# Performance work log

Hardware: AMD Instinct MI355X
Metric: run time of the kernel (lower is better)

The kernel has to match this reference:

```python
import jax, jax.numpy as jnp
from jax import lax
import numpy as np

B, T, F = 256, 2048, 12
EV_VOCAB, RS_VOCAB = 32, 8
EED, RED = 6, 3
H, K = 96, 3
D = F + EED + RED  # 21


def setup_inputs() -> dict:
    key = jax.random.key(0)
    ks = jax.random.split(key, 12)
    s = 0.05
    return {
        'seq': jax.random.normal(ks[0], (B, T, F), jnp.float32),
        'ev': jax.random.randint(ks[1], (B, T), 0, EV_VOCAB),
        'rs': jax.random.randint(ks[2], (B, T), 0, RS_VOCAB),
        'lengths': jax.random.randint(ks[3], (B,), 1, T + 1),  # valid lengths in [1, T]
        'event_emb': jax.random.normal(ks[4], (EV_VOCAB, EED), jnp.float32) * s,
        'result_emb': jax.random.normal(ks[5], (RS_VOCAB, RED), jnp.float32) * s,
        'W_ih': jax.random.normal(ks[6], (4 * H, D), jnp.float32) * s,
        'W_hh': jax.random.normal(ks[7], (4 * H, H), jnp.float32) * s,
        'b_ih': jnp.zeros((4 * H,), jnp.float32),
        'b_hh': jnp.zeros((4 * H,), jnp.float32),
        'W_mlp': jax.random.normal(ks[8], (H, H * K), jnp.float32) * s,
        'b_mlp': jnp.zeros((H,), jnp.float32),
        'W_fc': jax.random.normal(ks[9], (2, 2 * H), jnp.float32) * s,
        'b_fc': jnp.zeros((2,), jnp.float32),
    }


def reference(seq, ev, rs, lengths, event_emb, result_emb, W_ih, W_hh, b_ih, b_hh,
              W_mlp, b_mlp, W_fc, b_fc):
    # embed + concat -> [B,T,D]
    x = jnp.concatenate([seq, event_emb[ev], result_emb[rs]], axis=-1)
    xs = jnp.swapaxes(x, 0, 1)  # [T,B,D]
    ts = jnp.arange(T)
    b = b_ih + b_hh

    def step(carry, inp):
        h, c = carry
        x_t, t = inp
        gates = x_t @ W_ih.T + h @ W_hh.T + b  # [B,4H]
        i, f, g, o = jnp.split(gates, 4, axis=-1)  # PyTorch gate order i,f,g,o
        i = jax.nn.sigmoid(i); f = jax.nn.sigmoid(f)
        g = jnp.tanh(g); o = jax.nn.sigmoid(o)
        c_new = f * c + i * g
        h_new = o * jnp.tanh(c_new)
        m = (t < lengths)[:, None]  # packed-seq semantics: freeze state past length
        h = jnp.where(m, h_new, h)
        c = jnp.where(m, c_new, c)
        out = jnp.where(m, h_new, jnp.zeros_like(h_new))  # pad_packed zeros
        return (h, c), out

    h0 = jnp.zeros((B, H), x.dtype)
    (h_fin, _), outs = lax.scan(step, (h0, h0), (xs, ts))
    out_padded = jnp.swapaxes(outs, 0, 1)  # [B,T,H]

    # vectorized last-k gather (replaces torch Python loop)
    idx = lengths[:, None] - K + jnp.arange(K)  # [B,K]
    valid = idx >= 0
    gathered = jnp.take_along_axis(out_padded, jnp.clip(idx, 0)[:, :, None], axis=1)
    gathered = jnp.where(valid[:, :, None], gathered, jnp.zeros_like(gathered))
    lastk = gathered.reshape(B, K * H)

    h_lastk = jax.nn.relu(lastk @ W_mlp.T + b_mlp)
    h = jnp.concatenate([h_fin, h_lastk], axis=1)  # [B,2H]
    return h @ W_fc.T + b_fc  # [B,2]
```

## Files before the change

kernel.cpp:

```cpp
#include <hip/hip_runtime.h>

#define TT 2048
#define FF 12
#define HH 96
#define CH 128
#define L2E 1.44269504088896340736f

__device__ __forceinline__ float fast_exp2(float x){ return __builtin_amdgcn_exp2f(x); }
__device__ __forceinline__ float fast_rcp(float x){ return __builtin_amdgcn_rcpf(x); }

__global__ __launch_bounds__(512, 2) void lstm_persist(
  const float* __restrict__ seq, const int* __restrict__ ev, const int* __restrict__ rsi,
  const int* __restrict__ len, const float* __restrict__ eemb, const float* __restrict__ remb,
  const float* __restrict__ W_ih, const float* __restrict__ W_hh,
  const float* __restrict__ b_ih, const float* __restrict__ b_hh,
  const float* __restrict__ W_mlp, const float* __restrict__ b_mlp,
  const float* __restrict__ W_fc, const float* __restrict__ b_fc,
  float* __restrict__ out)
{
  const int b   = blockIdx.x;
  const int tid = threadIdx.x;
  const int w   = tid >> 6;
  const int l   = tid & 63;

  __shared__ __align__(16) float vh[HH];
  __shared__ __align__(16) float xch[CH][32];
  __shared__ __align__(16) float part[6*8*64];
  __shared__ __align__(16) float act[384];
  __shared__ __align__(16) float lastk[3*HH];
  __shared__ __align__(16) float h2[2*HH];
  __shared__ __align__(16) float et[32*6];
  __shared__ __align__(16) float rt[8*3];
  __shared__ int evb[CH];
  __shared__ int rsb[CH];

  float wreg[96];
  if (w < 6) {
    #pragma unroll
    for (int k = 0; k < 6; ++k) {
      const int g = l + 64*k;
      const float* p = W_hh + g*96 + 16*w;
      #pragma unroll
      for (int i = 0; i < 16; ++i) wreg[k*16+i] = p[i];
    }
  } else if (w == 6) {
    #pragma unroll
    for (int k = 0; k < 6; ++k) {
      const int g = l + 64*k;
      const float* p = W_ih + g*21;
      #pragma unroll
      for (int i = 0; i < 16; ++i) wreg[k*16+i] = p[i];
    }
  } else {
    #pragma unroll
    for (int k = 0; k < 6; ++k) {
      const int g = l + 64*k;
      #pragma unroll
      for (int i = 0; i < 16; ++i) {
        const int c = 16 + i;
        wreg[k*16+i] = (c < 21) ? W_ih[g*21 + c] : 0.f;
      }
    }
  }
  const float bg = (tid < 384) ? (b_ih[tid] + b_hh[tid]) : 0.f;

  for (int i = tid; i < HH;   i += 512) vh[i] = 0.f;
  for (int i = tid; i < 3*HH; i += 512) lastk[i] = 0.f;
  for (int i = tid; i < 192;  i += 512) et[i] = eemb[i];
  for (int i = tid; i < 24;   i += 512) rt[i] = remb[i];

  float c_state = 0.f;
  const int L = len[b];

  for (int t0 = 0; t0 < L; t0 += CH) {
    for (int q = tid; q < CH*FF; q += 512) {
      const int r = q / 12;
      const int c = q - r*12;
      xch[r][c] = seq[(size_t)b*(TT*FF) + (size_t)t0*FF + q];
    }
    if (tid < CH) {
      evb[tid] = ev [b*TT + t0 + tid];
      rsb[tid] = rsi[b*TT + t0 + tid];
    }
    __syncthreads();
    for (int q = tid; q < CH*20; q += 512) {
      const int r  = q / 20;
      const int cc = q - r*20 + 12;
      float val;
      if (cc < 18)      val = et[evb[r]*6 + (cc-12)];
      else if (cc < 21) val = rt[rsb[r]*3 + (cc-18)];
      else              val = 0.f;
      xch[r][cc] = val;
    }
    __syncthreads();

    const int nr = min(CH, L - t0);
    for (int r = 0; r < nr; ++r) {
      const float* sp = (w < 6) ? (vh + 16*w) : (&xch[r][16*(w-6)]);
      const float4 q0 = ((const float4*)sp)[0];
      const float4 q1 = ((const float4*)sp)[1];
      const float4 q2 = ((const float4*)sp)[2];
      const float4 q3 = ((const float4*)sp)[3];
      const float xv[16] = {q0.x,q0.y,q0.z,q0.w, q1.x,q1.y,q1.z,q1.w,
                            q2.x,q2.y,q2.z,q2.w, q3.x,q3.y,q3.z,q3.w};
      #pragma unroll
      for (int k = 0; k < 6; ++k) {
        float a = 0.f;
        #pragma unroll
        for (int i = 0; i < 16; ++i) a = fmaf(wreg[k*16+i], xv[i], a);
        part[(k*8 + w)*64 + l] = a;
      }
      __syncthreads();
      if (tid < 384) {
        float s = bg;
        const int kk = tid >> 6;
        const int ll = tid & 63;
        #pragma unroll
        for (int ww = 0; ww < 8; ++ww) s += part[(kk*8 + ww)*64 + ll];
        const bool is_t = (tid >= 192) && (tid < 288);
        const float arg = is_t ? (-2.f*L2E)*fabsf(s) : (-L2E)*s;
        const float e  = fast_exp2(arg);
        const float r1 = fast_rcp(1.f + e);
        const float th = copysignf((1.f - e) * r1, s);
        act[tid] = is_t ? th : r1;
      }
      __syncthreads();
      if (tid < 96) {
        const float i_ = act[tid];
        const float f_ = act[96  + tid];
        const float g_ = act[192 + tid];
        const float o_ = act[288 + tid];
        c_state = fmaf(f_, c_state, i_*g_);
        const float e  = fast_exp2((-2.f*L2E)*fabsf(c_state));
        const float th = copysignf((1.f - e) * fast_rcp(1.f + e), c_state);
        const float hn = o_ * th;
        vh[tid] = hn;
        const int kk = (t0 + r) + 3 - L;
        if (kk >= 0) lastk[kk*96 + tid] = hn;
      }
      __syncthreads();
    }
  }

  if (tid < 192) {
    const int hh = tid / 96;
    const int m  = tid - hh*96;
    const float* wp = W_mlp + m*288 + hh*144;
    const float* xp = lastk + hh*144;
    float s = 0.f;
    #pragma unroll 8
    for (int i = 0; i < 144; ++i) s = fmaf(wp[i], xp[i], s);
    act[tid] = s;
  }
  __syncthreads();
  if (tid < 96) {
    const float hl = act[tid] + act[96+tid] + b_mlp[tid];
    h2[96 + tid] = fmaxf(hl, 0.f);
    h2[tid] = vh[tid];
  }
  __syncthreads();
  if (tid < 128) {
    const int o  = tid >> 6;
    const int ll = tid & 63;
    const float* wf = W_fc + o*192 + 3*ll;
    float s = fmaf(wf[0], h2[3*ll+0], fmaf(wf[1], h2[3*ll+1], wf[2]*h2[3*ll+2]));
    #pragma unroll
    for (int off = 32; off > 0; off >>= 1) s += __shfl_down(s, off);
    if (ll == 0) out[b*2 + o] = s + b_fc[o];
  }
}

extern "C" void kernel_launch(void* const* d_in, const int* in_sizes, int n_in,
                              void* d_out, int out_size, void* d_ws, size_t ws_size,
                              hipStream_t stream) {
  const float* seq   = (const float*)d_in[0];
  const int*   ev    = (const int*)  d_in[1];
  const int*   rsi   = (const int*)  d_in[2];
  const int*   len   = (const int*)  d_in[3];
  const float* eemb  = (const float*)d_in[4];
  const float* remb  = (const float*)d_in[5];
  const float* W_ih  = (const float*)d_in[6];
  const float* W_hh  = (const float*)d_in[7];
  const float* b_ih  = (const float*)d_in[8];
  const float* b_hh  = (const float*)d_in[9];
  const float* W_mlp = (const float*)d_in[10];
  const float* b_mlp = (const float*)d_in[11];
  const float* W_fc  = (const float*)d_in[12];
  const float* b_fc  = (const float*)d_in[13];

  hipLaunchKernelGGL(lstm_persist, dim3(256), dim3(512), 0, stream,
                     seq, ev, rsi, len, eemb, remb, W_ih, W_hh, b_ih, b_hh,
                     W_mlp, b_mlp, W_fc, b_fc, (float*)d_out);
}
```

Baseline: 1.327 ms.

## Restructure LSTM step to one barrier using in-wave gate exchange and double-buffered h

Each thread now owns one gate row split across two half-waves, using 60 packed weights and f2 FMAs. Gate partial sums are combined with a shuffle, and the i/f/g/o activations are exchanged among lanes with shuffles. This replaces the shared-memory partial reduction and activation buffers and removes two of the three barriers per timestep. Double-buffering h avoids a read/write race with only one barrier per step, and the block grows to 768 threads. The cost is redundant cell-state computation across lanes.

```diff
diff --git a/kernel.cpp b/kernel.cpp
--- a/kernel.cpp
+++ b/kernel.cpp
@@ -4,12 +4,16 @@
 #define FF 12
 #define HH 96
 #define CH 128
+#define NT 768
 #define L2E 1.44269504088896340736f
+
+typedef __attribute__((ext_vector_type(2))) float f2;
+typedef __attribute__((ext_vector_type(4))) float f4;
 
 __device__ __forceinline__ float fast_exp2(float x){ return __builtin_amdgcn_exp2f(x); }
 __device__ __forceinline__ float fast_rcp(float x){ return __builtin_amdgcn_rcpf(x); }
 
-__global__ __launch_bounds__(512, 2) void lstm_persist(
+__global__ __launch_bounds__(NT, 3) void lstm_persist(
   const float* __restrict__ seq, const int* __restrict__ ev, const int* __restrict__ rsi,
   const int* __restrict__ len, const float* __restrict__ eemb, const float* __restrict__ remb,
   const float* __restrict__ W_ih, const float* __restrict__ W_hh,
@@ -22,58 +26,45 @@
   const int tid = threadIdx.x;
   const int w   = tid >> 6;
   const int l   = tid & 63;
+  const int kh  = l >> 5;
+  const int lh  = l & 31;
+  const int gt  = lh >> 3;
+  const int hq  = lh & 7;
+  const int ht  = 8*w + hq;
+  const int g   = gt*96 + ht;
 
-  __shared__ __align__(16) float vh[HH];
+  __shared__ __align__(16) float hbuf[2][96];
   __shared__ __align__(16) float xch[CH][32];
-  __shared__ __align__(16) float part[6*8*64];
-  __shared__ __align__(16) float act[384];
   __shared__ __align__(16) float lastk[3*HH];
+  __shared__ __align__(16) float tmp[192];
   __shared__ __align__(16) float h2[2*HH];
   __shared__ __align__(16) float et[32*6];
   __shared__ __align__(16) float rt[8*3];
   __shared__ int evb[CH];
   __shared__ int rsb[CH];
 
-  float wreg[96];
-  if (w < 6) {
-    #pragma unroll
-    for (int k = 0; k < 6; ++k) {
-      const int g = l + 64*k;
-      const float* p = W_hh + g*96 + 16*w;
-      #pragma unroll
-      for (int i = 0; i < 16; ++i) wreg[k*16+i] = p[i];
-    }
-  } else if (w == 6) {
-    #pragma unroll
-    for (int k = 0; k < 6; ++k) {
-      const int g = l + 64*k;
-      const float* p = W_ih + g*21;
-      #pragma unroll
-      for (int i = 0; i < 16; ++i) wreg[k*16+i] = p[i];
-    }
-  } else {
-    #pragma unroll
-    for (int k = 0; k < 6; ++k) {
-      const int g = l + 64*k;
-      #pragma unroll
-      for (int i = 0; i < 16; ++i) {
-        const int c = 16 + i;
-        wreg[k*16+i] = (c < 21) ? W_ih[g*21 + c] : 0.f;
-      }
-    }
+  f2 w2[30];
+  #pragma unroll
+  for (int j = 0; j < 30; ++j) {
+    float v0, v1;
+    const int c0 = kh*60 + 2*j;
+    v0 = (c0 < 96) ? W_hh[g*96 + c0] : ((c0 < 117) ? W_ih[g*21 + (c0-96)] : 0.f);
+    const int c1 = c0 + 1;
+    v1 = (c1 < 96) ? W_hh[g*96 + c1] : ((c1 < 117) ? W_ih[g*21 + (c1-96)] : 0.f);
+    w2[j] = (f2){v0, v1};
   }
-  const float bg = (tid < 384) ? (b_ih[tid] + b_hh[tid]) : 0.f;
+  const float bg = b_ih[g] + b_hh[g];
 
-  for (int i = tid; i < HH;   i += 512) vh[i] = 0.f;
-  for (int i = tid; i < 3*HH; i += 512) lastk[i] = 0.f;
-  for (int i = tid; i < 192;  i += 512) et[i] = eemb[i];
-  for (int i = tid; i < 24;   i += 512) rt[i] = remb[i];
+  for (int i = tid; i < 2*HH; i += NT) hbuf[0][i] = 0.f;
+  for (int i = tid; i < 3*HH; i += NT) lastk[i] = 0.f;
+  for (int i = tid; i < 192;  i += NT) et[i] = eemb[i];
+  for (int i = tid; i < 24;   i += NT) rt[i] = remb[i];
 
   float c_state = 0.f;
   const int L = len[b];
 
   for (int t0 = 0; t0 < L; t0 += CH) {
-    for (int q = tid; q < CH*FF; q += 512) {
+    for (int q = tid; q < CH*FF; q += NT) {
       const int r = q / 12;
       const int c = q - r*12;
       xch[r][c] = seq[(size_t)b*(TT*FF) + (size_t)t0*FF + q];
@@ -83,7 +74,7 @@
       rsb[tid] = rsi[b*TT + t0 + tid];
     }
     __syncthreads();
-    for (int q = tid; q < CH*20; q += 512) {
+    for (int q = tid; q < CH*20; q += NT) {
       const int r  = q / 20;
       const int cc = q - r*20 + 12;
       float val;
@@ -96,52 +87,59 @@
 
     const int nr = min(CH, L - t0);
     for (int r = 0; r < nr; ++r) {
-      const float* sp = (w < 6) ? (vh + 16*w) : (&xch[r][16*(w-6)]);
-      const float4 q0 = ((const float4*)sp)[0];
-      const float4 q1 = ((const float4*)sp)[1];
-      const float4 q2 = ((const float4*)sp)[2];
-      const float4 q3 = ((const float4*)sp)[3];
-      const float xv[16] = {q0.x,q0.y,q0.z,q0.w, q1.x,q1.y,q1.z,q1.w,
-                            q2.x,q2.y,q2.z,q2.w, q3.x,q3.y,q3.z,q3.w};
+      const int t   = t0 + r;
+      const int cur = t & 1;
+      const float* hb = &hbuf[cur][0];
+      const float* xr = &xch[r][0];
+      const f4* A  = (const f4*)(hb + kh*60);
+      const f4* Bv = kh ? (const f4*)xr : ((const f4*)hb) + 9;
+
+      f2 acc = (f2){0.f, 0.f};
       #pragma unroll
-      for (int k = 0; k < 6; ++k) {
-        float a = 0.f;
-        #pragma unroll
-        for (int i = 0; i < 16; ++i) a = fmaf(wreg[k*16+i], xv[i], a);
-        part[(k*8 + w)*64 + l] = a;
+      for (int j = 0; j < 9; ++j) {
+        const f4 q = A[j];
+        acc = w2[2*j]   * q.xy + acc;
+        acc = w2[2*j+1] * q.zw + acc;
       }
-      __syncthreads();
-      if (tid < 384) {
-        float s = bg;
-        const int kk = tid >> 6;
-        const int ll = tid & 63;
-        #pragma unroll
-        for (int ww = 0; ww < 8; ++ww) s += part[(kk*8 + ww)*64 + ll];
-        const bool is_t = (tid >= 192) && (tid < 288);
-        const float arg = is_t ? (-2.f*L2E)*fabsf(s) : (-L2E)*s;
-        const float e  = fast_exp2(arg);
-        const float r1 = fast_rcp(1.f + e);
-        const float th = copysignf((1.f - e) * r1, s);
-        act[tid] = is_t ? th : r1;
+      #pragma unroll
+      for (int j = 9; j < 15; ++j) {
+        const f4 q = Bv[j-9];
+        acc = w2[2*j]   * q.xy + acc;
+        acc = w2[2*j+1] * q.zw + acc;
       }
-      __syncthreads();
-      if (tid < 96) {
-        const float i_ = act[tid];
-        const float f_ = act[96  + tid];
-        const float g_ = act[192 + tid];
-        const float o_ = act[288 + tid];
-        c_state = fmaf(f_, c_state, i_*g_);
-        const float e  = fast_exp2((-2.f*L2E)*fabsf(c_state));
-        const float th = copysignf((1.f - e) * fast_rcp(1.f + e), c_state);
-        const float hn = o_ * th;
-        vh[tid] = hn;
-        const int kk = (t0 + r) + 3 - L;
-        if (kk >= 0) lastk[kk*96 + tid] = hn;
+      float p = acc.x + acc.y;
+      p += __shfl_xor(p, 32);
+      const float s = p + bg;
+
+      const bool is_t = (gt == 2);
+      const float arg = is_t ? (-2.f*L2E)*fabsf(s) : (-L2E)*s;
+      const float e   = fast_exp2(arg);
+      const float r1  = fast_rcp(1.f + e);
+      const float a0  = is_t ? copysignf((1.f - e)*r1, s) : r1;
+
+      const float a1 = __shfl_xor(a0, 8);
+      const float a2 = __shfl_xor(a0, 16);
+      const float a3 = __shfl_xor(a0, 24);
+      const float gi = (gt==0) ? a0 : (gt==1) ? a1 : (gt==2) ? a2 : a3;
+      const float gf = (gt==1) ? a0 : (gt==0) ? a1 : (gt==3) ? a2 : a3;
+      const float gg = (gt==2) ? a0 : (gt==3) ? a1 : (gt==0) ? a2 : a3;
+      const float go = (gt==3) ? a0 : (gt==2) ? a1 : (gt==1) ? a2 : a3;
+
+      c_state = fmaf(gf, c_state, gi*gg);
+      const float e2 = fast_exp2((-2.f*L2E)*fabsf(c_state));
+      const float th = copysignf((1.f - e2)*fast_rcp(1.f + e2), c_state);
+      const float hn = go * th;
+
+      if (l < 8) {
+        hbuf[cur ^ 1][ht] = hn;
+        const int kk = t + 3 - L;
+        if (kk >= 0) lastk[kk*96 + ht] = hn;
       }
       __syncthreads();
     }
   }
 
+  const float* hfin = &hbuf[L & 1][0];
   if (tid < 192) {
     const int hh = tid / 96;
     const int m  = tid - hh*96;
@@ -150,13 +148,13 @@
     float s = 0.f;
     #pragma unroll 8
     for (int i = 0; i < 144; ++i) s = fmaf(wp[i], xp[i], s);
-    act[tid] = s;
+    tmp[tid] = s;
   }
   __syncthreads();
   if (tid < 96) {
-    const float hl = act[tid] + act[96+tid] + b_mlp[tid];
+    const float hl = tmp[tid] + tmp[96+tid] + b_mlp[tid];
     h2[96 + tid] = fmaxf(hl, 0.f);
-    h2[tid] = vh[tid];
+    h2[tid] = hfin[tid];
   }
   __syncthreads();
   if (tid < 128) {
@@ -188,7 +186,7 @@
   const float* W_fc  = (const float*)d_in[12];
   const float* b_fc  = (const float*)d_in[13];
 
-  hipLaunchKernelGGL(lstm_persist, dim3(256), dim3(512), 0, stream,
+  hipLaunchKernelGGL(lstm_persist, dim3(256), dim3(NT), 0, stream,
                      seq, ev, rsi, len, eemb, remb, W_ih, W_hh, b_ih, b_hh,
                      W_mlp, b_mlp, W_fc, b_fc, (float*)d_out);
 }
```

New measurement: 1.427 ms. +7.5%, slower.
